# Kernel optimization log

Measured on AMD Instinct MI355X. Metric: run time of the kernel, lower is better.

Reference implementation:

```python
import jax, jax.numpy as jnp
import numpy as np
import math

B, S, D, H, L = 8, 1024, 768, 12, 3
DK = D // H

def setup_inputs() -> dict:
    key = jax.random.key(0)
    ks = jax.random.split(key, 12)
    std = math.sqrt(1.0 / D)
    inp = {
        'Q': jax.random.normal(ks[0], (B, S, D), jnp.float32),
        'K': jax.random.normal(ks[1], (B, S, D), jnp.float32),
        'V': jax.random.normal(ks[2], (B, S, D), jnp.float32),
        'dist': jax.random.uniform(ks[3], (B, S, S), jnp.float32),
        # stacked per-layer torch.nn.Linear params: weight [out,in], bias [out]
        'Wq': jax.random.normal(ks[4], (L, D, D), jnp.float32) * std,
        'bq': jnp.zeros((L, D), jnp.float32),
        'Wk': jax.random.normal(ks[5], (L, D, D), jnp.float32) * std,
        'bk': jnp.zeros((L, D), jnp.float32),
        'Wv': jax.random.normal(ks[6], (L, D, D), jnp.float32) * std,
        'bv': jnp.zeros((L, D), jnp.float32),
        'Wo': jax.random.normal(ks[7], (L, D, D), jnp.float32) * std,
        'bo': jnp.zeros((L, D), jnp.float32),
    }
    return inp

def reference(Q, K, V, dist, Wq, bq, Wk, bk, Wv, bv, Wo, bo):
    scale = math.sqrt(DK)
    # adjacency with self loops, broadcast over heads: [B,1,S,S]
    mask = (dist + jnp.eye(S, dtype=dist.dtype))[:, None, :, :]
    input_value = V
    for i in range(L):
        q = (Q @ Wq[i].T + bq[i]).reshape(B, S, H, DK).transpose(0, 2, 1, 3)
        k = (K @ Wk[i].T + bk[i]).reshape(B, S, H, DK).transpose(0, 2, 1, 3)
        v = (V @ Wv[i].T + bv[i]).reshape(B, S, H, DK).transpose(0, 2, 1, 3)
        scores = jnp.einsum('bhqd,bhkd->bhqk', q, k) / scale
        attn = jax.nn.softmax(scores, axis=-1) * mask  # post-softmax multiply
        ctx = jnp.einsum('bhqk,bhkd->bhqd', attn, v)
        ctx = ctx.transpose(0, 2, 1, 3).reshape(B, S, D)
        out = ctx @ Wo[i].T + bo[i]
        K = V = out
    return V + input_value
```

## Files before the change

kernel.cpp:

```cpp
#include <hip/hip_runtime.h>
#include <hip/hip_bf16.h>


typedef unsigned short u16;
typedef unsigned long long u64;
typedef __attribute__((ext_vector_type(8))) short short8;
typedef __attribute__((ext_vector_type(4))) float floatx4;
typedef __attribute__((ext_vector_type(16))) float floatx16;
typedef __attribute__((ext_vector_type(4))) unsigned uintx4;

#define NB 8
#define NS 1024
#define ND 768
#define NH 12
#define NDK 64
#define NM (NB * NS)
#define WELEM (ND * ND)
#define ACT ((size_t)NM * ND)

static __device__ __forceinline__ u16 f2bf(float f) {
  union { float f; unsigned u; } x; x.f = f;
  unsigned r = x.u + 0x7fffu + ((x.u >> 16) & 1u);
  return (u16)(r >> 16);
}
static __device__ __forceinline__ float u2f(unsigned u) {
  union { unsigned u; float f; } x; x.u = u;
  return x.f;
}
static __device__ __forceinline__ unsigned f2u(float f) {
  union { float f; unsigned u; } x; x.f = f;
  return x.u;
}
static __device__ __forceinline__ float fexp2(float x) {
#if __has_builtin(__builtin_amdgcn_exp2f)
  return __builtin_amdgcn_exp2f(x);
#else
  return exp2f(x);
#endif
}

typedef __attribute__((address_space(1))) void gvoid;
typedef __attribute__((address_space(3))) void lvoid;
static __device__ __forceinline__ void gl_lds16(const void* g, void* l) {
  __builtin_amdgcn_global_load_lds((gvoid*)g, (lvoid*)l, 16, 0, 0);
}


__global__ void cvt_qkv_kernel(const float* __restrict__ Q, const float* __restrict__ K,
                               const float* __restrict__ V, u16* __restrict__ dst) {
  int z = blockIdx.y;
  const float* s = (z == 0) ? Q : (z == 1 ? K : V);
  size_t i = ((size_t)blockIdx.x * 256 + threadIdx.x) * 4;
  float4 v = *(const float4*)(s + i);
  u64 pk = (u64)f2bf(v.x) | ((u64)f2bf(v.y) << 16) | ((u64)f2bf(v.z) << 32) |
           ((u64)f2bf(v.w) << 48);
  *(u64*)(dst + (size_t)z * ACT + i) = pk;
}

__global__ void cvt_w_all_kernel(const float* __restrict__ Wq, const float* __restrict__ Wk,
                                 const float* __restrict__ Wv, const float* __restrict__ Wo2,
                                 u16* __restrict__ Wqb, u16* __restrict__ wkv,
                                 u16* __restrict__ Wob2) {
  int z = blockIdx.y;
  size_t i = ((size_t)blockIdx.x * 256 + threadIdx.x) * 4;
  const float* src;
  u16* dst;
  if (z < 3) {
    src = Wq + (size_t)z * WELEM; dst = Wqb + (size_t)z * WELEM;
  } else if (z < 6) {
    int k = z - 3;
    src = Wk + (size_t)k * WELEM; dst = wkv + (size_t)(2 * k) * WELEM;
  } else if (z < 9) {
    int k = z - 6;
    src = Wv + (size_t)k * WELEM; dst = wkv + (size_t)(2 * k + 1) * WELEM;
  } else {
    src = Wo2; dst = Wob2;
  }
  float4 v = *(const float4*)(src + i);
  u64 pk = (u64)f2bf(v.x) | ((u64)f2bf(v.y) << 16) | ((u64)f2bf(v.z) << 32) |
           ((u64)f2bf(v.w) << 48);
  *(u64*)(dst + i) = pk;
}

__global__ void wot_kernel(const float* __restrict__ Wo, u16* __restrict__ WoT) {
  __shared__ float tile[32][33];
  int z = blockIdx.z;
  int bm = blockIdx.y * 32, bi = blockIdx.x * 32;
  int tx = threadIdx.x & 31, ty = threadIdx.x >> 5;
  const float* src = Wo + (size_t)z * WELEM;
  u16* dst = WoT + (size_t)z * WELEM;
#pragma unroll
  for (int r = 0; r < 4; r++)
    tile[ty + 8 * r][tx] = src[(size_t)(bm + ty + 8 * r) * ND + bi + tx];
  __syncthreads();
#pragma unroll
  for (int r = 0; r < 4; r++)
    dst[(size_t)(bi + ty + 8 * r) * ND + bm + tx] = f2bf(tile[tx][ty + 8 * r]);
}

__global__ void mask_cvt_kernel(const float* __restrict__ dist, u16* __restrict__ dst) {
  int i = (blockIdx.x * 256 + threadIdx.x) * 4;
  float4 v = *(const float4*)(dist + i);
  int b = i >> 20;
  int q = (i >> 10) & 1023;
  int k = i & 1023;
  float a0 = v.x + (q == k ? 1.f : 0.f);
  float a1 = v.y + (q == k + 1 ? 1.f : 0.f);
  float a2 = v.z + (q == k + 2 ? 1.f : 0.f);
  float a3 = v.w + (q == k + 3 ? 1.f : 0.f);
  u64 pk = (u64)f2bf(a0) | ((u64)f2bf(a1) << 16) | ((u64)f2bf(a2) << 32) |
           ((u64)f2bf(a3) << 48);
  size_t o = ((((size_t)b * 8 + (q >> 7)) * 8 + (k >> 7)) << 14) + ((q & 127) << 7) + (k & 127);
  *(u64*)(dst + o) = pk;
}


enum { MODE_QALL = 0, MODE_KV0 = 1, MODE_KV2 = 2, MODE_COMB = 3, MODE_FINAL = 4 };

template <int MODE>
__global__ __launch_bounds__(256, 3) void gemm_bt_kernel(const u16* __restrict__ A,
                                                         const u16* __restrict__ W,
                                                         void* __restrict__ outp,
                                                         const float* __restrict__ resid) {
  __shared__ u16 As[128 * 64];
  __shared__ u16 Bs[128 * 64];
  if (MODE == MODE_KV0) {
    A += (size_t)blockIdx.z * ACT;
    W += (size_t)blockIdx.z * WELEM;
  }
  if (MODE == MODE_COMB) {
    A += (size_t)blockIdx.z * WELEM;
    W += (size_t)(blockIdx.z >> 1) * WELEM;
  }
  const int t = threadIdx.x;
  const int l = t & 63;
  const int w = t >> 6;
  const int wm = w >> 1, wn = w & 1;
  const int quad = l >> 4, l15 = l & 15;
  const int m0 = blockIdx.y * 128;
  const int n0 = blockIdx.x * 128;

  const int srow_l = w * 8 + (l >> 3);
  const int schunk = (l & 7) ^ ((w * 4 + (l >> 4)) & 7);
  const u16* pa = A + (size_t)(m0 + srow_l) * ND + schunk * 8;
  const u16* pb = W + (size_t)(n0 + srow_l) * ND + schunk * 8;
  u16* lAw = &As[(size_t)(w * 8) * 64];
  u16* lBw = &Bs[(size_t)(w * 8) * 64];

  const int fswz = (l15 >> 1) & 7;

  floatx4 acc[4][4];
#pragma unroll
  for (int mi = 0; mi < 4; mi++)
#pragma unroll
    for (int ni = 0; ni < 4; ni++) acc[mi][ni] = floatx4{0.f, 0.f, 0.f, 0.f};

  for (int k0 = 0; k0 < ND; k0 += 64) {
    __syncthreads();
#pragma unroll
    for (int j = 0; j < 4; j++) {
      gl_lds16(pa + k0 + (size_t)j * 32 * ND, lAw + j * 32 * 64);
      gl_lds16(pb + k0 + (size_t)j * 32 * ND, lBw + j * 32 * 64);
    }
    __syncthreads();

#pragma unroll
    for (int h = 0; h < 2; h++) {
      const int fsw = (((h * 4 + quad) ^ fswz) & 7) << 3;
      short8 af[4], bf[4];
#pragma unroll
      for (int mi = 0; mi < 4; mi++)
        af[mi] = *(const short8*)&As[(wm * 64 + mi * 16 + l15) * 64 + fsw];
#pragma unroll
      for (int ni = 0; ni < 4; ni++)
        bf[ni] = *(const short8*)&Bs[(wn * 64 + ni * 16 + l15) * 64 + fsw];
#pragma unroll
      for (int mi = 0; mi < 4; mi++)
#pragma unroll
        for (int ni = 0; ni < 4; ni++)
          acc[mi][ni] =
              __builtin_amdgcn_mfma_f32_16x16x32_bf16(af[mi], bf[ni], acc[mi][ni], 0, 0, 0);
    }
  }

#pragma unroll
  for (int mi = 0; mi < 4; mi++) {
#pragma unroll
    for (int ni = 0; ni < 4; ni++) {
      const int mb = m0 + wm * 64 + mi * 16 + quad * 4;
      const int n = n0 + wn * 64 + ni * 16 + l15;
      if (MODE == MODE_QALL) {
        const float QSCALE = 0.18033688011112042f;
        int lay = n / ND, rr = n % ND;
        int hh = rr >> 6, dk = rr & 63;
#pragma unroll
        for (int r = 0; r < 4; r++) {
          int m = mb + r, bb = m >> 10, ss = m & 1023;
          ((u16*)outp)[((((size_t)lay * NB + bb) * NH + hh) * NS + ss) * NDK + dk] =
              f2bf(acc[mi][ni][r] * QSCALE);
        }
      } else if (MODE == MODE_KV0 || MODE == MODE_KV2) {
        const bool isV = (MODE == MODE_KV0) ? (blockIdx.z == 1) : (n >= ND);
        const int nn = (MODE == MODE_KV2 && n >= ND) ? n - ND : n;
        const int hh = nn >> 6, dk = nn & 63;
        u16* ob = (u16*)outp +
                  ((MODE == MODE_KV0) ? (size_t)blockIdx.z * ACT : (isV ? ACT : (size_t)0));
        if (!isV) {
#pragma unroll
          for (int r = 0; r < 4; r++) {
            int m = mb + r, bb = m >> 10, ss = m & 1023;
            ob[(((size_t)bb * NH + hh) * NS + ss) * NDK + dk] = f2bf(acc[mi][ni][r]);
          }
        } else {
          int bb = mb >> 10, ss = mb & 1023;
          u64 pk = (u64)f2bf(acc[mi][ni][0]) | ((u64)f2bf(acc[mi][ni][1]) << 16) |
                   ((u64)f2bf(acc[mi][ni][2]) << 32) | ((u64)f2bf(acc[mi][ni][3]) << 48);
          *(u64*)&ob[(((size_t)bb * NH + hh) * NDK + dk) * NS + ss] = pk;
        }
      } else if (MODE == MODE_COMB) {
        u16* ob = (u16*)outp + (size_t)blockIdx.z * WELEM;
#pragma unroll
        for (int r = 0; r < 4; r++) ob[(size_t)(mb + r) * ND + n] = f2bf(acc[mi][ni][r]);
      } else {
#pragma unroll
        for (int r = 0; r < 4; r++) {
          size_t idx = (size_t)(mb + r) * ND + n;
          ((float*)outp)[idx] = acc[mi][ni][r] + resid[idx];
        }
      }
    }
  }
}

__global__ __launch_bounds__(256, 3) void attn_kernel(const u16* __restrict__ qact,
                                                      const u16* __restrict__ kact,
                                                      const u16* __restrict__ vact,
                                                      const u16* __restrict__ maskb,
                                                      u16* __restrict__ ctx) {
  __shared__ u16 ks[128 * 64];
  __shared__ u16 vts[64 * 128];

  const int pid = blockIdx.x;
  const int b = pid & 7;
  const int slot = pid >> 3;
  const int h = slot % NH;
  const int qt = slot / NH;
  const int t = threadIdx.x;
  const int l = t & 63, w = t >> 6;
  const int l31 = l & 31, lh = l >> 5;
  const int qrow = w * 32 + l31;
  const int kk7 = l31 & 7;

  const size_t bh = (size_t)(b * NH + h);
  const u16* qg = qact + (bh * NS + qt * 128) * NDK;
  const u16* kg = kact + bh * NS * NDK;
  const u16* vg = vact + bh * NDK * NS;
  const u16* mbase = maskb + ((((size_t)b * 8 + qt) * 8) << 14) + ((size_t)qrow << 7) + lh * 4;

  short8 qf[4];
#pragma unroll
  for (int s4 = 0; s4 < 4; s4++)
    qf[s4] = *(const short8*)(qg + (size_t)qrow * NDK + (2 * s4 + lh) * 8);

  const int kg_swz = (l & 7) ^ (l >> 3);
  const u16* pk_g = kg + (size_t)(w * 32 + (l >> 3)) * NDK + kg_swz * 8;
  u16* lK = &ks[(size_t)w * 32 * NDK];
  const int vr_l = l >> 4;
  const int vg_swz0 = (l & 15) ^ vr_l;
  const int vg_swz1 = (l & 15) ^ (vr_l + 4);
  const u16* pv_g = vg + (size_t)(w * 16 + vr_l) * NS;
  u16* lV = &vts[(size_t)w * 4 * 512];

  float m_run = -1e30f, l_run = 0.f;
  floatx16 o_acc[2];
#pragma unroll
  for (int di = 0; di < 2; di++)
#pragma unroll
    for (int r = 0; r < 16; r++) o_acc[di][r] = 0.f;

  for (int kt = 0; kt < 8; kt++) {
    __syncthreads();
#pragma unroll
    for (int j = 0; j < 4; j++) {
      gl_lds16(pk_g + (size_t)(kt * 128 + j * 8) * NDK, lK + j * 512);
      gl_lds16(pv_g + (size_t)j * 4 * NS + kt * 128 + (j & 1 ? vg_swz1 : vg_swz0) * 8,
               lV + j * 512);
    }
    __syncthreads();

    floatx16 sacc[4];
#pragma unroll
    for (int ni = 0; ni < 4; ni++)
#pragma unroll
      for (int r = 0; r < 16; r++) sacc[ni][r] = 0.f;

#pragma unroll
    for (int s4 = 0; s4 < 4; s4++) {
#pragma unroll
      for (int ni = 0; ni < 4; ni++) {
        int krow = ni * 32 + l31;
        short8 kf = *(const short8*)&ks[krow * 64 + (((2 * s4 + lh) ^ kk7) << 3)];
        sacc[ni] = __builtin_amdgcn_mfma_f32_32x32x16_bf16(kf, qf[s4], sacc[ni], 0, 0, 0);
      }
    }

    uint2 mu[16];
    {
      const u16* mt = mbase + ((size_t)kt << 14);
#pragma unroll
      for (int ni = 0; ni < 4; ni++)
#pragma unroll
        for (int rq = 0; rq < 4; rq++)
          mu[ni * 4 + rq] = *(const uint2*)(mt + ni * 32 + rq * 8);
    }

    float mx = -1e30f;
#pragma unroll
    for (int ni = 0; ni < 4; ni++)
#pragma unroll
      for (int r = 0; r < 16; r++) mx = fmaxf(mx, sacc[ni][r]);
    mx = fmaxf(mx, __shfl_xor(mx, 32));
    float mnew = fmaxf(m_run, mx);
    float alpha = fexp2(m_run - mnew);
    float ssum = 0.f;
#pragma unroll
    for (int ni = 0; ni < 4; ni++)
#pragma unroll
      for (int r = 0; r < 16; r++) {
        float p = fexp2(sacc[ni][r] - mnew);
        sacc[ni][r] = p;
        ssum += p;
      }
    ssum += __shfl_xor(ssum, 32);
    m_run = mnew;
    l_run = l_run * alpha + ssum;
#pragma unroll
    for (int di = 0; di < 2; di++)
#pragma unroll
      for (int r = 0; r < 16; r++) o_acc[di][r] *= alpha;

#pragma unroll
    for (int ni = 0; ni < 4; ni++) {
      unsigned pkl[8];
#pragma unroll
      for (int rq = 0; rq < 4; rq++) {
        uint2 m2 = mu[ni * 4 + rq];
        float p0 = sacc[ni][rq * 4 + 0] * u2f(m2.x << 16);
        float p1 = sacc[ni][rq * 4 + 1] * u2f(m2.x & 0xffff0000u);
        float p2 = sacc[ni][rq * 4 + 2] * u2f(m2.y << 16);
        float p3 = sacc[ni][rq * 4 + 3] * u2f(m2.y & 0xffff0000u);
        pkl[rq * 2] = __builtin_amdgcn_perm(f2u(p1), f2u(p0), 0x07060302u);
        pkl[rq * 2 + 1] = __builtin_amdgcn_perm(f2u(p3), f2u(p2), 0x07060302u);
      }
#pragma unroll
      for (int sh = 0; sh < 2; sh++) {
        const int Ax = sh * 4, Bx = Ax + 2;
        unsigned u0 = lh ? pkl[Ax] : pkl[Bx];
        unsigned u1 = lh ? pkl[Ax + 1] : pkl[Bx + 1];
        unsigned su0 = (unsigned)__shfl_xor((int)u0, 32);
        unsigned su1 = (unsigned)__shfl_xor((int)u1, 32);
        unsigned v0 = lh ? pkl[Bx] : pkl[Ax];
        unsigned v1 = lh ? pkl[Bx + 1] : pkl[Ax + 1];
        uintx4 bbv;
        bbv.x = lh ? su0 : v0;
        bbv.y = lh ? su1 : v1;
        bbv.z = lh ? v0 : su0;
        bbv.w = lh ? v1 : su1;
        short8 pfrag = __builtin_bit_cast(short8, bbv);
        const int chunk = 2 * (ni * 2 + sh) + lh;
#pragma unroll
        for (int di = 0; di < 2; di++) {
          int vrow = di * 32 + l31;
          short8 vf = *(const short8*)&vts[vrow * 128 + ((chunk ^ kk7) << 3)];
          o_acc[di] = __builtin_amdgcn_mfma_f32_32x32x16_bf16(vf, pfrag, o_acc[di], 0, 0, 0);
        }
      }
    }
  }

  float inv = 1.0f / l_run;
  u16* crow = ctx + ((size_t)b * NS + qt * 128 + qrow) * ND + h * NDK;
#pragma unroll
  for (int di = 0; di < 2; di++) {
#pragma unroll
    for (int rq = 0; rq < 4; rq++) {
      int d = di * 32 + rq * 8 + lh * 4;
      u64 pk4 = (u64)f2bf(o_acc[di][rq * 4 + 0] * inv) |
                ((u64)f2bf(o_acc[di][rq * 4 + 1] * inv) << 16) |
                ((u64)f2bf(o_acc[di][rq * 4 + 2] * inv) << 32) |
                ((u64)f2bf(o_acc[di][rq * 4 + 3] * inv) << 48);
      *(u64*)(crow + d) = pk4;
    }
  }
}


extern "C" void kernel_launch(void* const* d_in, const int* in_sizes, int n_in, void* d_out,
                              int out_size, void* d_ws, size_t ws_size, hipStream_t stream) {
  (void)in_sizes; (void)n_in; (void)out_size; (void)ws_size;
  const float* Qf = (const float*)d_in[0];
  const float* Kf = (const float*)d_in[1];
  const float* Vf = (const float*)d_in[2];
  const float* dist = (const float*)d_in[3];
  const float* Wq = (const float*)d_in[4];
  const float* Wk = (const float*)d_in[6];
  const float* Wv = (const float*)d_in[8];
  const float* Wo = (const float*)d_in[10];

  u16* p = (u16*)d_ws;
  u16* Qb = p;    p += ACT;
  u16* Kb = p;    p += ACT;
  u16* Vb = p;    p += ACT;
  u16* Wqb = p;   p += 3 * (size_t)WELEM;
  u16* wkv = p;   p += 6 * (size_t)WELEM;
  u16* Wob2 = p;  p += (size_t)WELEM;
  u16* WoTb = p;  p += 2 * (size_t)WELEM;
  u16* comb = p;  p += 4 * (size_t)WELEM;
  u16* maskb = p; p += (size_t)NB * NS * NS;
  u16* qact = p;  p += 3 * ACT;
  u16* kact = p;  p += ACT;
  u16* vact = p;  p += ACT;
  u16* ctxb = p;  p += ACT;

  cvt_qkv_kernel<<<dim3(ACT / 1024, 3), 256, 0, stream>>>(Qf, Kf, Vf, Qb);
  cvt_w_all_kernel<<<dim3(WELEM / 1024, 10), 256, 0, stream>>>(
      Wq, Wk, Wv, Wo + 2 * (size_t)WELEM, Wqb, wkv, Wob2);
  wot_kernel<<<dim3(24, 24, 2), 256, 0, stream>>>(Wo, WoTb);
  mask_cvt_kernel<<<dim3((NB * NS * NS) / 1024), 256, 0, stream>>>(dist, maskb);

  gemm_bt_kernel<MODE_COMB><<<dim3(6, 6, 4), 256, 0, stream>>>(wkv + 2 * (size_t)WELEM, WoTb,
                                                               comb, nullptr);
  gemm_bt_kernel<MODE_QALL><<<dim3(18, 64), 256, 0, stream>>>(Qb, Wqb, qact, nullptr);

  gemm_bt_kernel<MODE_KV0><<<dim3(6, 64, 2), 256, 0, stream>>>(Kb, wkv, kact, nullptr);
  attn_kernel<<<dim3(768), 256, 0, stream>>>(qact, kact, vact, maskb, ctxb);
  gemm_bt_kernel<MODE_KV2><<<dim3(12, 64), 256, 0, stream>>>(ctxb, comb, kact, nullptr);
  attn_kernel<<<dim3(768), 256, 0, stream>>>(qact + ACT, kact, vact, maskb, ctxb);
  gemm_bt_kernel<MODE_KV2><<<dim3(12, 64), 256, 0, stream>>>(ctxb, comb + 2 * (size_t)WELEM,
                                                             kact, nullptr);
  attn_kernel<<<dim3(768), 256, 0, stream>>>(qact + 2 * ACT, kact, vact, maskb, ctxb);
  gemm_bt_kernel<MODE_FINAL><<<dim3(6, 64), 256, 0, stream>>>(ctxb, Wob2, (void*)d_out, Vf);
}
```

Before: 541.3 us.

## Drop online softmax max tracking, prefetch mask loads, add mask L2 warm kernel

The attention kernel no longer tracks a running row maximum or rescales the output accumulator. It exponentiates the scores directly and sums them into a per-lane partial, which is reduced once at the end. The per-tile mask loads are issued before the barrier so they overlap the K/V staging. A new kernel streams the bf16 mask through the cache before the first attention launch. Removing max subtraction saves the reductions, shuffles and rescale multiplies, but risks exp overflow when scores are large, and the warm kernel costs an extra launch and a full pass over memory.

```diff
diff --git a/kernel.cpp b/kernel.cpp
--- a/kernel.cpp
+++ b/kernel.cpp
@@ -114,6 +114,19 @@
   *(u64*)(dst + o) = pk;
 }
 
+__global__ void mask_warm_kernel(const u16* __restrict__ maskb) {
+  const int pid = blockIdx.x;
+  const int b = pid & 7;
+  const int slot = pid >> 3;
+  const float4* bb = (const float4*)(maskb + (size_t)b * NS * NS);
+  const int nvec = NS * NS / 8;
+  int i = slot * 256 + threadIdx.x;
+  for (; i < nvec; i += 96 * 256) {
+    float4 v = bb[i];
+    asm volatile("" ::"v"(v.x), "v"(v.y), "v"(v.z), "v"(v.w));
+  }
+}
+
 
 enum { MODE_QALL = 0, MODE_KV0 = 1, MODE_KV2 = 2, MODE_COMB = 3, MODE_FINAL = 4 };
 
@@ -271,7 +284,7 @@
   const u16* pv_g = vg + (size_t)(w * 16 + vr_l) * NS;
   u16* lV = &vts[(size_t)w * 4 * 512];
 
-  float m_run = -1e30f, l_run = 0.f;
+  float l_part = 0.f;
   floatx16 o_acc[2];
 #pragma unroll
   for (int di = 0; di < 2; di++)
@@ -285,6 +298,15 @@
       gl_lds16(pk_g + (size_t)(kt * 128 + j * 8) * NDK, lK + j * 512);
       gl_lds16(pv_g + (size_t)j * 4 * NS + kt * 128 + (j & 1 ? vg_swz1 : vg_swz0) * 8,
                lV + j * 512);
+    }
+    uint2 mu[16];
+    {
+      const u16* mt = mbase + ((size_t)kt << 14);
+#pragma unroll
+      for (int ni = 0; ni < 4; ni++)
+#pragma unroll
+        for (int rq = 0; rq < 4; rq++)
+          mu[ni * 4 + rq] = *(const uint2*)(mt + ni * 32 + rq * 8);
     }
     __syncthreads();
 
@@ -304,51 +326,21 @@
       }
     }
 
-    uint2 mu[16];
-    {
-      const u16* mt = mbase + ((size_t)kt << 14);
-#pragma unroll
-      for (int ni = 0; ni < 4; ni++)
-#pragma unroll
-        for (int rq = 0; rq < 4; rq++)
-          mu[ni * 4 + rq] = *(const uint2*)(mt + ni * 32 + rq * 8);
-    }
-
-    float mx = -1e30f;
-#pragma unroll
-    for (int ni = 0; ni < 4; ni++)
-#pragma unroll
-      for (int r = 0; r < 16; r++) mx = fmaxf(mx, sacc[ni][r]);
-    mx = fmaxf(mx, __shfl_xor(mx, 32));
-    float mnew = fmaxf(m_run, mx);
-    float alpha = fexp2(m_run - mnew);
-    float ssum = 0.f;
-#pragma unroll
-    for (int ni = 0; ni < 4; ni++)
-#pragma unroll
-      for (int r = 0; r < 16; r++) {
-        float p = fexp2(sacc[ni][r] - mnew);
-        sacc[ni][r] = p;
-        ssum += p;
-      }
-    ssum += __shfl_xor(ssum, 32);
-    m_run = mnew;
-    l_run = l_run * alpha + ssum;
-#pragma unroll
-    for (int di = 0; di < 2; di++)
-#pragma unroll
-      for (int r = 0; r < 16; r++) o_acc[di][r] *= alpha;
-
 #pragma unroll
     for (int ni = 0; ni < 4; ni++) {
       unsigned pkl[8];
 #pragma unroll
       for (int rq = 0; rq < 4; rq++) {
         uint2 m2 = mu[ni * 4 + rq];
-        float p0 = sacc[ni][rq * 4 + 0] * u2f(m2.x << 16);
-        float p1 = sacc[ni][rq * 4 + 1] * u2f(m2.x & 0xffff0000u);
-        float p2 = sacc[ni][rq * 4 + 2] * u2f(m2.y << 16);
-        float p3 = sacc[ni][rq * 4 + 3] * u2f(m2.y & 0xffff0000u);
+        float e0 = fexp2(sacc[ni][rq * 4 + 0]);
+        float e1 = fexp2(sacc[ni][rq * 4 + 1]);
+        float e2 = fexp2(sacc[ni][rq * 4 + 2]);
+        float e3 = fexp2(sacc[ni][rq * 4 + 3]);
+        l_part += (e0 + e1) + (e2 + e3);
+        float p0 = e0 * u2f(m2.x << 16);
+        float p1 = e1 * u2f(m2.x & 0xffff0000u);
+        float p2 = e2 * u2f(m2.y << 16);
+        float p3 = e3 * u2f(m2.y & 0xffff0000u);
         pkl[rq * 2] = __builtin_amdgcn_perm(f2u(p1), f2u(p0), 0x07060302u);
         pkl[rq * 2 + 1] = __builtin_amdgcn_perm(f2u(p3), f2u(p2), 0x07060302u);
       }
@@ -378,6 +370,7 @@
     }
   }
 
+  float l_run = l_part + __shfl_xor(l_part, 32);
   float inv = 1.0f / l_run;
   u16* crow = ctx + ((size_t)b * NS + qt * 128 + qrow) * ND + h * NDK;
 #pragma unroll
@@ -433,6 +426,7 @@
   gemm_bt_kernel<MODE_QALL><<<dim3(18, 64), 256, 0, stream>>>(Qb, Wqb, qact, nullptr);
 
   gemm_bt_kernel<MODE_KV0><<<dim3(6, 64, 2), 256, 0, stream>>>(Kb, wkv, kact, nullptr);
+  mask_warm_kernel<<<dim3(768), 256, 0, stream>>>(maskb);
   attn_kernel<<<dim3(768), 256, 0, stream>>>(qact, kact, vact, maskb, ctxb);
   gemm_bt_kernel<MODE_KV2><<<dim3(12, 64), 256, 0, stream>>>(ctxb, comb, kact, nullptr);
   attn_kernel<<<dim3(768), 256, 0, stream>>>(qact + ACT, kact, vact, maskb, ctxb);
```

Measured after the change: 553.6 us. 1.02x slower.
